# Kernel tuning notes

Hardware: AMD Instinct MI355X
Metric: run time of the kernel (lower is better)

## Reference

```python
import jax, jax.numpy as jnp
import numpy as np

B, C, MID, OUT, T, N = 8, 128, 64, 128, 4, 512


def setup_inputs() -> dict:
    key = jax.random.key(0)
    ks = jax.random.split(key, 5)
    def w(k, o, i, scale):
        return (jax.random.normal(k, (o, i), jnp.float32) * scale)
    return {
        "pc": jax.random.normal(ks[0], (B, C, T, N), jnp.float32),
        "theta_w": w(ks[1], MID, C, 0.05), "theta_b": jnp.zeros((MID,), jnp.float32),
        "phi_w": w(ks[2], MID, C, 0.05), "phi_b": jnp.zeros((MID,), jnp.float32),
        "g_w": w(ks[3], MID, C, 0.05), "g_b": jnp.zeros((MID,), jnp.float32),
        "refine_w": w(ks[4], OUT, MID, 0.05), "refine_b": jnp.zeros((OUT,), jnp.float32),
    }


def reference(pc, theta_w, theta_b, phi_w, phi_b, g_w, g_b, refine_w, refine_b):
    b, c, t, n = pc.shape
    tn = t * n
    # pt_utils.Conv2d with bn=False: 1x1 conv + bias + ReLU
    def proj(wt, bs):
        h = jnp.einsum('oc,bctn->botn', wt, pc) + bs[None, :, None, None]
        return jax.nn.relu(h).reshape(b, -1, tn)  # [B, mid, TN]

    theta = proj(theta_w, theta_b).transpose(0, 2, 1)  # [B, TN, mid]
    phi = proj(phi_w, phi_b)                            # [B, mid, TN]
    g = proj(g_w, g_b).transpose(0, 2, 1)               # [B, TN, mid]

    scores = jnp.einsum('bqm,bmk->bqk', theta, phi)     # [B, TN, TN]
    corr = jax.nn.softmax(scores, axis=1)               # softmax over QUERY axis (dim=1)
    y = jnp.einsum('bqk,bkm->bmq', corr, g)             # bmm then transpose(1,2): [B, mid, TN]

    # pt_utils.Conv1d with bn=False: 1x1 conv + bias + ReLU
    refined = jax.nn.relu(jnp.einsum('om,bmq->boq', refine_w, y) + refine_b[None, :, None])
    # faithful raw reshape (row-major, same as torch) then permute, plus residual
    z = refined.reshape(b, t, n, -1).transpose(0, 3, 1, 2) + pc
    return z
```

## Files before the change

kernel.cpp:

```cpp
#include <hip/hip_runtime.h>


constexpr int NL75_TN  = 2048;
constexpr int NL75_MID = 64;
constexpr int NL75_C   = 128;
constexpr float NL75_L2E = 1.4426950408889634f;

typedef __attribute__((ext_vector_type(8))) short nl75_bf8;
typedef __attribute__((ext_vector_type(4))) float nl75_f4;

__device__ __forceinline__ unsigned short nl75_f2b(float f) {
  unsigned x = __float_as_uint(f);
  return (unsigned short)((x + 0x7fffu + ((x >> 16) & 1u)) >> 16);
}

__device__ __forceinline__ unsigned int nl75_pkbf16(float lo, float hi) {
  unsigned int r;
  asm("v_cvt_pk_bf16_f32 %0, %1, %2" : "=v"(r) : "v"(lo), "v"(hi));
  return r;
}

__device__ __forceinline__ float nl75_exp2(float x) {
  float r;
  asm("v_exp_f32 %0, %1" : "=v"(r) : "v"(x));
  return r;
}

typedef const __attribute__((address_space(1))) unsigned int* nl75_gp;
typedef __attribute__((address_space(3))) unsigned int* nl75_lp;
__device__ __forceinline__ void nl75_gld16(const void* g, void* l) {
  __builtin_amdgcn_global_load_lds((nl75_gp)g, (nl75_lp)l, 16, 0, 0);
}

__device__ __forceinline__ void nl75_stage64(const unsigned short* src,
                                             size_t pitch, unsigned short* lds,
                                             int tid) {
  const int w = tid >> 6, lane = tid & 63;
#pragma unroll
  for (int r = 0; r < 2; r++) {
    const int slot = r * 256 + w * 64 + lane;
    const int row = slot >> 3, x = slot & 7;
    const unsigned short* s =
        src + (size_t)row * pitch + ((x * 8) ^ ((row & 7) << 3));
    nl75_gld16(s, lds + (size_t)(r * 256 + w * 64) * 8);
  }
}

__global__ void NonLocalLayer_75771813036638_kernel() {}

__global__ void nl75_proj(const float* pc, const float* w0, const float* b0,
                          const float* w1, const float* b1, const float* w2,
                          const float* b2, unsigned short* thT,
                          unsigned short* phT, unsigned short* gN, int bOff,
                          int nb) {
  __shared__ float wT[NL75_C][68];
  const int bl = blockIdx.x, pj = blockIdx.y, qt = blockIdx.z;
  const int b = bOff + bl;
  const float* wp = (pj == 0) ? w0 : (pj == 1) ? w1 : w2;
  const float* bp = (pj == 0) ? b0 : (pj == 1) ? b1 : b2;
  const int tid = threadIdx.x;
  for (int i = tid; i < NL75_MID * NL75_C; i += 256)
    wT[i & 127][i >> 7] = wp[i];
  __syncthreads();
  const int qg = tid & 31, mg = tid >> 5;
  const int q = qt * 64 + qg * 2, m0 = mg * 8;
  const float* pcb = pc + (long long)b * NL75_C * NL75_TN + q;
  float acc[8][2];
#pragma unroll
  for (int i = 0; i < 8; i++) acc[i][0] = acc[i][1] = bp[m0 + i];
#pragma unroll 4
  for (int c = 0; c < NL75_C; c++) {
    const float2 p = *(const float2*)&pcb[(size_t)c * NL75_TN];
    float w8[8];
    *(float4*)&w8[0] = *(const float4*)&wT[c][m0];
    *(float4*)&w8[4] = *(const float4*)&wT[c][m0 + 4];
#pragma unroll
    for (int i = 0; i < 8; i++) {
      acc[i][0] = fmaf(w8[i], p.x, acc[i][0]);
      acc[i][1] = fmaf(w8[i], p.y, acc[i][1]);
    }
  }
  if (pj < 2) {
    unsigned int u[8];
#pragma unroll
    for (int i = 0; i < 4; i++) {
      u[i] = nl75_pkbf16(fmaxf(acc[2 * i][0], 0.0f),
                         fmaxf(acc[2 * i + 1][0], 0.0f));
      u[4 + i] = nl75_pkbf16(fmaxf(acc[2 * i][1], 0.0f),
                             fmaxf(acc[2 * i + 1][1], 0.0f));
    }
    unsigned short* dst =
        (pj == 0 ? thT : phT) + ((size_t)bl * NL75_TN + q) * 64 + m0;
    *reinterpret_cast<uint4*>(dst) = *reinterpret_cast<uint4*>(&u[0]);
    *reinterpret_cast<uint4*>(dst + 64) = *reinterpret_cast<uint4*>(&u[4]);
  } else {
#pragma unroll
    for (int i = 0; i < 8; i++) {
      ushort2 v;
      v.x = nl75_f2b(fmaxf(acc[i][0], 0.0f));
      v.y = nl75_f2b(fmaxf(acc[i][1], 0.0f));
      *(ushort2*)&gN[((size_t)bl * NL75_MID + m0 + i) * NL75_TN + q] = v;
    }
  }
}

__global__ void nl75_stats(const unsigned short* thT, const unsigned short* phT,
                           float* Sp, int nb, int qsplit) {
  __shared__ unsigned short thL[2][64 * 64];
  const int bl = blockIdx.x;
  const int kt = blockIdx.y & 31, qs = blockIdx.y >> 5;
  const int tid = threadIdx.x, lane = tid & 63, w = tid >> 6;
  const int l15 = lane & 15, quad = lane >> 4;
  const int k0 = kt * 64;
  const unsigned short* thB = thT + (size_t)bl * NL75_TN * 64;
  const unsigned short* phB = phT + (size_t)bl * NL75_TN * 64;
  const size_t kr = (size_t)(k0 + w * 16 + l15) * 64;
  const nl75_bf8 b0 = *(const nl75_bf8*)&phB[kr + quad * 8];
  const nl75_bf8 b1 = *(const nl75_bf8*)&phB[kr + 32 + quad * 8];
  const int qtN = 32 / qsplit, qtBeg = qs * qtN;
  nl75_stage64(thB + (size_t)(qtBeg * 64) * 64, 64, thL[0], tid);
  __syncthreads();
  float S = 0.0f;
  for (int qt = qtBeg; qt < qtBeg + qtN; qt++) {
    const int cur = (qt - qtBeg) & 1;
    if (qt + 1 < qtBeg + qtN)
      nl75_stage64(thB + (size_t)((qt + 1) * 64) * 64, 64, thL[cur ^ 1], tid);
    __builtin_amdgcn_s_setprio(1);
#pragma unroll
    for (int q16 = 0; q16 < 4; q16++) {
      const int qr = q16 * 16 + l15;
      const int sw = (qr & 7) << 3;
      const nl75_bf8 a0 = *(const nl75_bf8*)&thL[cur][qr * 64 + ((quad * 8) ^ sw)];
      const nl75_bf8 a1 =
          *(const nl75_bf8*)&thL[cur][qr * 64 + ((32 + quad * 8) ^ sw)];
      nl75_f4 c = {0.0f, 0.0f, 0.0f, 0.0f};
      c = __builtin_amdgcn_mfma_f32_16x16x32_bf16(a0, b0, c, 0, 0, 0);
      c = __builtin_amdgcn_mfma_f32_16x16x32_bf16(a1, b1, c, 0, 0, 0);
      const float e0 = nl75_exp2(c[0] * NL75_L2E) + nl75_exp2(c[1] * NL75_L2E);
      const float e1 = nl75_exp2(c[2] * NL75_L2E) + nl75_exp2(c[3] * NL75_L2E);
      S += e0 + e1;
    }
    __builtin_amdgcn_s_setprio(0);
    __syncthreads();
  }
  S += __shfl_xor(S, 16);
  S += __shfl_xor(S, 32);
  if (quad == 0) {
    const long long base = ((long long)(qs * nb + bl)) * NL75_TN + k0;
    Sp[base + w * 16 + l15] = S;
  }
}

__global__ void nl75_attn(const unsigned short* thT, const unsigned short* phT,
                          const unsigned short* gN, const float* Sp,
                          float* yPart, int nb, int ksplit, int qsplit) {
  __shared__ unsigned short phL[2][64 * 64];
  __shared__ unsigned short gL[2][64 * 64];
  __shared__ float ekL[2048];
  const int wg = blockIdx.x;
  const int bl = wg % nb;
  const int rest = wg / nb;
  const int qt = rest & 15, ks = rest >> 4;
  const int tid = threadIdx.x, lane = tid & 63, w = tid >> 6;
  const int l15 = lane & 15, quad = lane >> 4;
  const int q0 = qt * 128;
  const unsigned short* thB = thT + (size_t)bl * NL75_TN * 64;
  const unsigned short* phB = phT + (size_t)bl * NL75_TN * 64;
  const unsigned short* gB = gN + (size_t)bl * NL75_MID * NL75_TN;
  const int ktN = 32 / ksplit;
  const int ktBeg = ks * ktN, ktEnd = ktBeg + ktN;
  nl75_stage64(phB + (size_t)(ktBeg * 64) * 64, 64, phL[0], tid);
  nl75_stage64(gB + ktBeg * 64, NL75_TN, gL[0], tid);
  nl75_bf8 aq[2][2];
#pragma unroll
  for (int s = 0; s < 2; s++) {
    const size_t qr = (size_t)(q0 + s * 64 + w * 16 + l15) * 64;
    aq[s][0] = *(const nl75_bf8*)&thB[qr + quad * 8];
    aq[s][1] = *(const nl75_bf8*)&thB[qr + 32 + quad * 8];
  }
  const int kRange = ktN * 64;
  for (int kk = tid; kk < kRange; kk += 256) {
    const int k = ktBeg * 64 + kk;
    float S = 0.0f;
    for (int qs = 0; qs < qsplit; qs++)
      S += Sp[((size_t)(qs * nb + bl)) * NL75_TN + k];
    ekL[kk] = __log2f(S);
  }
  nl75_f4 yacc[2][4];
#pragma unroll
  for (int s = 0; s < 2; s++)
#pragma unroll
    for (int i = 0; i < 4; i++) yacc[s][i] = (nl75_f4){0.0f, 0.0f, 0.0f, 0.0f};
  __syncthreads();
  union Frag { nl75_bf8 h; unsigned int u[4]; };
  for (int kt = ktBeg; kt < ktEnd; kt++) {
    const int cur = (kt - ktBeg) & 1;
    if (kt + 1 < ktEnd) {
      nl75_stage64(phB + (size_t)((kt + 1) * 64) * 64, 64, phL[cur ^ 1], tid);
      nl75_stage64(gB + (kt + 1) * 64, NL75_TN, gL[cur ^ 1], tid);
    }
    const int ekBase = (kt - ktBeg) * 64;
    nl75_f4 ek[4];
#pragma unroll
    for (int t = 0; t < 4; t++)
      ek[t] = *(const nl75_f4*)&ekL[ekBase + t * 16 + quad * 4];
    __builtin_amdgcn_s_setprio(1);
    unsigned int pk[2][8];
#pragma unroll
    for (int t = 0; t < 4; t++) {
      const int krr = t * 16 + l15;
      const int sw = (krr & 7) << 3;
      const nl75_bf8 b0 =
          *(const nl75_bf8*)&phL[cur][krr * 64 + ((quad * 8) ^ sw)];
      const nl75_bf8 b1 =
          *(const nl75_bf8*)&phL[cur][krr * 64 + ((32 + quad * 8) ^ sw)];
#pragma unroll
      for (int s = 0; s < 2; s++) {
        nl75_f4 c = {0.0f, 0.0f, 0.0f, 0.0f};
        c = __builtin_amdgcn_mfma_f32_16x16x32_bf16(b0, aq[s][0], c, 0, 0, 0);
        c = __builtin_amdgcn_mfma_f32_16x16x32_bf16(b1, aq[s][1], c, 0, 0, 0);
        pk[s][t * 2 + 0] =
            nl75_pkbf16(nl75_exp2(fmaf(c[0], NL75_L2E, -ek[t][0])),
                        nl75_exp2(fmaf(c[1], NL75_L2E, -ek[t][1])));
        pk[s][t * 2 + 1] =
            nl75_pkbf16(nl75_exp2(fmaf(c[2], NL75_L2E, -ek[t][2])),
                        nl75_exp2(fmaf(c[3], NL75_L2E, -ek[t][3])));
      }
    }
#pragma unroll
    for (int mtile = 0; mtile < 4; mtile++) {
      const int m = mtile * 16 + l15;
      const int sw = (m & 7) << 3;
      const unsigned short* row = &gL[cur][m * 64];
      Frag bg0, bg1;
      *(uint2*)&bg0.u[0] = *(const uint2*)&row[(quad * 4) ^ sw];
      *(uint2*)&bg0.u[2] = *(const uint2*)&row[(16 + quad * 4) ^ sw];
      *(uint2*)&bg1.u[0] = *(const uint2*)&row[(32 + quad * 4) ^ sw];
      *(uint2*)&bg1.u[2] = *(const uint2*)&row[(48 + quad * 4) ^ sw];
#pragma unroll
      for (int s = 0; s < 2; s++) {
        Frag a0, a1;
        a0.u[0] = pk[s][0]; a0.u[1] = pk[s][1];
        a0.u[2] = pk[s][2]; a0.u[3] = pk[s][3];
        a1.u[0] = pk[s][4]; a1.u[1] = pk[s][5];
        a1.u[2] = pk[s][6]; a1.u[3] = pk[s][7];
        yacc[s][mtile] = __builtin_amdgcn_mfma_f32_16x16x32_bf16(
            a0.h, bg0.h, yacc[s][mtile], 0, 0, 0);
        yacc[s][mtile] = __builtin_amdgcn_mfma_f32_16x16x32_bf16(
            a1.h, bg1.h, yacc[s][mtile], 0, 0, 0);
      }
    }
    __builtin_amdgcn_s_setprio(0);
    __syncthreads();
  }
  float* yB = yPart + ((size_t)(ks * nb + bl) * NL75_MID) * NL75_TN;
#pragma unroll
  for (int s = 0; s < 2; s++)
#pragma unroll
    for (int mtile = 0; mtile < 4; mtile++) {
      float4 v = make_float4(yacc[s][mtile][0], yacc[s][mtile][1],
                             yacc[s][mtile][2], yacc[s][mtile][3]);
      *(float4*)&yB[(size_t)(mtile * 16 + l15) * NL75_TN + q0 + s * 64 +
                    w * 16 + quad * 4] = v;
    }
}

__global__ void nl75_yred(const float* yPart, float* y, int nb, int ksplit) {
  const size_t tot = (size_t)nb * NL75_MID * NL75_TN / 4;
  const size_t stride = tot;
  const float4* src = (const float4*)yPart;
  float4* dst = (float4*)y;
  for (size_t i = (size_t)blockIdx.x * 256 + threadIdx.x; i < tot;
       i += (size_t)gridDim.x * 256) {
    float4 a = src[i];
    for (int ks = 1; ks < ksplit; ks++) {
      float4 b = src[(size_t)ks * stride + i];
      a.x += b.x; a.y += b.y; a.z += b.z; a.w += b.w;
    }
    dst[i] = a;
  }
}

__global__ void nl75_refsc(const float* yIn, const float* rW, const float* rB,
                           const float* pc, float* outP, int bOff, int nb,
                           int ksplit) {
  __shared__ float rwS[32][66];
  __shared__ float yS[NL75_MID][132];
  const int bl = blockIdx.x, cg = blockIdx.y, t = blockIdx.z;
  const int b = bOff + bl, c0 = cg * 8, tid = threadIdx.x;
  for (int i = tid; i < 32 * NL75_MID; i += 256) {
    int oh = i >> 6, m = i & 63;
    rwS[oh][m] = rW[(long long)(t * 32 + oh) * NL75_MID + m];
  }
  if (ksplit == 1) {
    const float* yB0 = yIn + (size_t)bl * NL75_MID * NL75_TN;
    for (int i = tid; i < NL75_MID * 32; i += 256) {
      int m = i >> 5, r = i & 31;
      int i16 = r >> 1, half = r & 1;
      const float4 v = *(const float4*)&yB0[(size_t)m * NL75_TN + i16 * 128 +
                                            c0 + half * 4];
      *(float4*)&yS[m][i16 * 8 + half * 4] = v;
    }
  } else {
    for (int i = tid; i < NL75_MID * 128; i += 256) {
      int m = i >> 7, qi = i & 127;
      int i16 = qi >> 3, cl = qi & 7;
      long long off = (long long)m * NL75_TN + i16 * 128 + c0 + cl;
      float v = 0.0f;
      for (int ks = 0; ks < ksplit; ks++)
        v += yIn[((long long)(ks * nb + bl) * NL75_MID) * NL75_TN + off];
      yS[m][qi] = v;
    }
  }
  __syncthreads();
  const int oh0 = (tid >> 5) * 4;
  const int q4 = (tid & 31) * 4;
  float acc[4][4];
#pragma unroll
  for (int i = 0; i < 4; i++) {
    float bias = rB[t * 32 + oh0 + i];
#pragma unroll
    for (int j = 0; j < 4; j++) acc[i][j] = bias;
  }
  for (int m = 0; m < NL75_MID; m++) {
    float yv[4];
#pragma unroll
    for (int j = 0; j < 4; j++) yv[j] = yS[m][q4 + j];
#pragma unroll
    for (int i = 0; i < 4; i++) {
      float w = rwS[oh0 + i][m];
#pragma unroll
      for (int j = 0; j < 4; j++) acc[i][j] = fmaf(w, yv[j], acc[i][j]);
    }
  }
  __syncthreads();
  float* outS = &yS[0][0];
  const int NP = 516;
#pragma unroll
  for (int i = 0; i < 4; i++) {
    const int oh = oh0 + i;
#pragma unroll
    for (int j = 0; j < 4; j++) {
      const int qi = q4 + j;
      outS[(qi & 7) * NP + oh * 16 + (qi >> 3)] = fmaxf(acc[i][j], 0.0f);
    }
  }
  __syncthreads();
  const size_t obase = (((size_t)b * 128 + c0) * 4 + t) * 512;
#pragma unroll
  for (int ii = 0; ii < 4; ii++) {
    const int fi = ii * 256 + tid;
    const int cl = fi >> 7, n0 = (fi & 127) * 4;
    float4 v = *(const float4*)&outS[cl * NP + n0];
    const size_t gi = obase + (size_t)cl * 4 * 512 + n0;
    const float4 p = *(const float4*)&pc[gi];
    v.x += p.x; v.y += p.y; v.z += p.z; v.w += p.w;
    *(float4*)&outP[gi] = v;
  }
}

extern "C" void kernel_launch(void* const* d_in, const int* in_sizes, int n_in,
                              void* d_out, int out_size, void* d_ws, size_t ws_size,
                              hipStream_t stream) {
  const float* pc = (const float*)d_in[0];
  const float* tw = (const float*)d_in[1];
  const float* tb = (const float*)d_in[2];
  const float* pw = (const float*)d_in[3];
  const float* pb = (const float*)d_in[4];
  const float* gw = (const float*)d_in[5];
  const float* gb = (const float*)d_in[6];
  const float* rw = (const float*)d_in[7];
  const float* rb = (const float*)d_in[8];
  float* out = (float*)d_out;

  const size_t yPB = (size_t)NL75_MID * NL75_TN;
  auto need = [&](int nb, int qs, int ks) -> size_t {
    return (3ull * nb * NL75_TN * 64 * 2) +
           ((size_t)qs * nb * NL75_TN + ((size_t)ks * nb + nb) * yPB) * 4;
  };

  int nb, qsplit, ksplit;
  if (ws_size >= need(8, 8, 8))      { nb = 8; qsplit = 8; ksplit = 8; }
  else if (ws_size >= need(8, 1, 1)) { nb = 8; qsplit = 1; ksplit = 1; }
  else                               { nb = 1; qsplit = 1; ksplit = 1; }
  const int nloop = 8 / nb;

  unsigned short* thT = (unsigned short*)d_ws;
  unsigned short* phT = thT + (size_t)nb * NL75_TN * 64;
  unsigned short* gN = phT + (size_t)nb * NL75_TN * 64;
  float* Sp = (float*)(gN + (size_t)nb * NL75_MID * NL75_TN);
  float* yPart = Sp + (size_t)qsplit * nb * NL75_TN;
  float* yFull = (ksplit > 1) ? yPart + (size_t)ksplit * nb * yPB : yPart;

  for (int l = 0; l < nloop; l++) {
    const int bOff = l * nb;
    nl75_proj<<<dim3(nb, 3, 32), 256, 0, stream>>>(pc, tw, tb, pw, pb, gw, gb,
                                                   thT, phT, gN, bOff, nb);
    nl75_stats<<<dim3(nb, 32 * qsplit), 256, 0, stream>>>(thT, phT, Sp, nb,
                                                          qsplit);
    nl75_attn<<<dim3(16 * ksplit * nb), 256, 0, stream>>>(
        thT, phT, gN, Sp, yPart, nb, ksplit, qsplit);
    if (ksplit > 1) {
      nl75_yred<<<dim3(1024), 256, 0, stream>>>(yPart, yFull, nb, ksplit);
      nl75_refsc<<<dim3(nb, 16, 4), 256, 0, stream>>>(yFull, rw, rb, pc, out,
                                                      bOff, nb, 1);
    } else {
      nl75_refsc<<<dim3(nb, 16, 4), 256, 0, stream>>>(yPart, rw, rb, pc, out,
                                                      bOff, nb, 1);
    }
  }
}
```

Measured before the change: 138.3 us.

## Double key tile per stats block and permute g layout for 128-bit LDS reads

The stats kernel now processes 128 keys per workgroup instead of 64, so each staged theta tile in LDS feeds twice as many MFMAs and the grid is halved. Separately, the projection kernel writes g in a permuted key order within each 64-key block, which lets the attention kernel fetch its B fragments with two 128-bit LDS loads instead of four 64-bit loads. The permutation has to match the MFMA K-lane ordering exactly or results will be wrong. Halving the stats grid also reduces parallelism and raises register use per thread.

```diff
diff --git a/kernel.cpp b/kernel.cpp
--- a/kernel.cpp
+++ b/kernel.cpp
@@ -94,12 +94,16 @@
     *reinterpret_cast<uint4*>(dst) = *reinterpret_cast<uint4*>(&u[0]);
     *reinterpret_cast<uint4*>(dst + 64) = *reinterpret_cast<uint4*>(&u[4]);
   } else {
+    const int kin = q & 63;
+    const int np = (kin >> 5) * 32 + (((kin & 15) >> 2) << 3) +
+                   (((kin >> 4) & 1) << 2) + (kin & 3);
+    const size_t gq = (size_t)(q & ~63) | np;
 #pragma unroll
     for (int i = 0; i < 8; i++) {
       ushort2 v;
       v.x = nl75_f2b(fmaxf(acc[i][0], 0.0f));
       v.y = nl75_f2b(fmaxf(acc[i][1], 0.0f));
-      *(ushort2*)&gN[((size_t)bl * NL75_MID + m0 + i) * NL75_TN + q] = v;
+      *(ushort2*)&gN[((size_t)bl * NL75_MID + m0 + i) * NL75_TN + gq] = v;
     }
   }
 }
@@ -108,19 +112,22 @@
                            float* Sp, int nb, int qsplit) {
   __shared__ unsigned short thL[2][64 * 64];
   const int bl = blockIdx.x;
-  const int kt = blockIdx.y & 31, qs = blockIdx.y >> 5;
+  const int kt = blockIdx.y & 15, qs = blockIdx.y >> 4;
   const int tid = threadIdx.x, lane = tid & 63, w = tid >> 6;
   const int l15 = lane & 15, quad = lane >> 4;
-  const int k0 = kt * 64;
+  const int k0 = kt * 128;
   const unsigned short* thB = thT + (size_t)bl * NL75_TN * 64;
   const unsigned short* phB = phT + (size_t)bl * NL75_TN * 64;
-  const size_t kr = (size_t)(k0 + w * 16 + l15) * 64;
-  const nl75_bf8 b0 = *(const nl75_bf8*)&phB[kr + quad * 8];
-  const nl75_bf8 b1 = *(const nl75_bf8*)&phB[kr + 32 + quad * 8];
+  const size_t kra = (size_t)(k0 + w * 16 + l15) * 64;
+  const size_t krb = (size_t)(k0 + 64 + w * 16 + l15) * 64;
+  const nl75_bf8 b0a = *(const nl75_bf8*)&phB[kra + quad * 8];
+  const nl75_bf8 b1a = *(const nl75_bf8*)&phB[kra + 32 + quad * 8];
+  const nl75_bf8 b0b = *(const nl75_bf8*)&phB[krb + quad * 8];
+  const nl75_bf8 b1b = *(const nl75_bf8*)&phB[krb + 32 + quad * 8];
   const int qtN = 32 / qsplit, qtBeg = qs * qtN;
   nl75_stage64(thB + (size_t)(qtBeg * 64) * 64, 64, thL[0], tid);
   __syncthreads();
-  float S = 0.0f;
+  float Sa = 0.0f, Sb = 0.0f;
   for (int qt = qtBeg; qt < qtBeg + qtN; qt++) {
     const int cur = (qt - qtBeg) & 1;
     if (qt + 1 < qtBeg + qtN)
@@ -133,21 +140,28 @@
       const nl75_bf8 a0 = *(const nl75_bf8*)&thL[cur][qr * 64 + ((quad * 8) ^ sw)];
       const nl75_bf8 a1 =
           *(const nl75_bf8*)&thL[cur][qr * 64 + ((32 + quad * 8) ^ sw)];
-      nl75_f4 c = {0.0f, 0.0f, 0.0f, 0.0f};
-      c = __builtin_amdgcn_mfma_f32_16x16x32_bf16(a0, b0, c, 0, 0, 0);
-      c = __builtin_amdgcn_mfma_f32_16x16x32_bf16(a1, b1, c, 0, 0, 0);
-      const float e0 = nl75_exp2(c[0] * NL75_L2E) + nl75_exp2(c[1] * NL75_L2E);
-      const float e1 = nl75_exp2(c[2] * NL75_L2E) + nl75_exp2(c[3] * NL75_L2E);
-      S += e0 + e1;
+      nl75_f4 ca = {0.0f, 0.0f, 0.0f, 0.0f};
+      ca = __builtin_amdgcn_mfma_f32_16x16x32_bf16(a0, b0a, ca, 0, 0, 0);
+      ca = __builtin_amdgcn_mfma_f32_16x16x32_bf16(a1, b1a, ca, 0, 0, 0);
+      nl75_f4 cb = {0.0f, 0.0f, 0.0f, 0.0f};
+      cb = __builtin_amdgcn_mfma_f32_16x16x32_bf16(a0, b0b, cb, 0, 0, 0);
+      cb = __builtin_amdgcn_mfma_f32_16x16x32_bf16(a1, b1b, cb, 0, 0, 0);
+      Sa += (nl75_exp2(ca[0] * NL75_L2E) + nl75_exp2(ca[1] * NL75_L2E)) +
+            (nl75_exp2(ca[2] * NL75_L2E) + nl75_exp2(ca[3] * NL75_L2E));
+      Sb += (nl75_exp2(cb[0] * NL75_L2E) + nl75_exp2(cb[1] * NL75_L2E)) +
+            (nl75_exp2(cb[2] * NL75_L2E) + nl75_exp2(cb[3] * NL75_L2E));
     }
     __builtin_amdgcn_s_setprio(0);
     __syncthreads();
   }
-  S += __shfl_xor(S, 16);
-  S += __shfl_xor(S, 32);
+  Sa += __shfl_xor(Sa, 16);
+  Sa += __shfl_xor(Sa, 32);
+  Sb += __shfl_xor(Sb, 16);
+  Sb += __shfl_xor(Sb, 32);
   if (quad == 0) {
     const long long base = ((long long)(qs * nb + bl)) * NL75_TN + k0;
-    Sp[base + w * 16 + l15] = S;
+    Sp[base + w * 16 + l15] = Sa;
+    Sp[base + 64 + w * 16 + l15] = Sb;
   }
 }
 
@@ -233,10 +247,8 @@
       const int sw = (m & 7) << 3;
       const unsigned short* row = &gL[cur][m * 64];
       Frag bg0, bg1;
-      *(uint2*)&bg0.u[0] = *(const uint2*)&row[(quad * 4) ^ sw];
-      *(uint2*)&bg0.u[2] = *(const uint2*)&row[(16 + quad * 4) ^ sw];
-      *(uint2*)&bg1.u[0] = *(const uint2*)&row[(32 + quad * 4) ^ sw];
-      *(uint2*)&bg1.u[2] = *(const uint2*)&row[(48 + quad * 4) ^ sw];
+      bg0.h = *(const nl75_bf8*)&row[(quad * 8) ^ sw];
+      bg1.h = *(const nl75_bf8*)&row[(32 + quad * 8) ^ sw];
 #pragma unroll
       for (int s = 0; s < 2; s++) {
         Frag a0, a1;
@@ -396,7 +408,7 @@
     const int bOff = l * nb;
     nl75_proj<<<dim3(nb, 3, 32), 256, 0, stream>>>(pc, tw, tb, pw, pb, gw, gb,
                                                    thT, phT, gN, bOff, nb);
-    nl75_stats<<<dim3(nb, 32 * qsplit), 256, 0, stream>>>(thT, phT, Sp, nb,
+    nl75_stats<<<dim3(nb, 16 * qsplit), 256, 0, stream>>>(thT, phT, Sp, nb,
                                                           qsplit);
     nl75_attn<<<dim3(16 * ksplit * nb), 256, 0, stream>>>(
         thT, phT, gN, Sp, yPart, nb, ksplit, qsplit);
```

Measured after the change: 139.3 us. About the same (+0.7%).
